# Performance work log

Hardware: AMD Instinct MI355X
Metric: run time of the kernel (lower is better)

The kernel has to match this reference:

```python
import jax, jax.numpy as jnp
import numpy as np

N, E = 100000, 1600000
D_IN, D_HID, D_OUT = 128, 128, 64


def setup_inputs() -> dict:
    key = jax.random.key(0)
    ks = jax.random.split(key, 12)
    x = jax.random.normal(ks[0], (N, D_IN), dtype=jnp.float32)
    edge_index = jax.random.randint(ks[1], (2, E), 0, N, dtype=jnp.int32)

    def glorot(k, fan_in, fan_out):
        lim = np.sqrt(6.0 / (fan_in + fan_out)).astype(np.float32)
        return jax.random.uniform(k, (fan_in, fan_out), jnp.float32, -lim, lim)

    return {
        "x": x,
        "edge_index": edge_index,
        "W_l0": glorot(ks[2], D_IN, D_HID), "W_r0": glorot(ks[3], D_IN, D_HID), "b0": jnp.zeros((D_HID,), jnp.float32),
        "W_l1": glorot(ks[4], D_HID, D_HID), "W_r1": glorot(ks[5], D_HID, D_HID), "b1": jnp.zeros((D_HID,), jnp.float32),
        "W_l2": glorot(ks[6], D_HID, D_OUT), "W_r2": glorot(ks[7], D_HID, D_OUT), "b2": jnp.zeros((D_OUT,), jnp.float32),
    }


def _sage_conv(x, src, dst, W_l, W_r, b):
    # mean aggregation of source features onto destination nodes
    msg = jnp.take(x, src, axis=0)                               # [E, d]
    agg = jax.ops.segment_sum(msg, dst, num_segments=N)          # [N, d]
    deg = jax.ops.segment_sum(jnp.ones_like(dst, x.dtype), dst, num_segments=N)
    agg = agg / jnp.maximum(deg, 1.0)[:, None]
    # out = lin_l(aggr) + lin_r(x); lin_l has bias (PyG SAGEConv convention)
    return agg @ W_l + x @ W_r + b


def reference(x, edge_index, W_l0, W_r0, b0, W_l1, W_r1, b1, W_l2, W_r2, b2):
    src, dst = edge_index[0], edge_index[1]
    h = jax.nn.relu(_sage_conv(x, src, dst, W_l0, W_r0, b0))
    h = jax.nn.relu(_sage_conv(h, src, dst, W_l1, W_r1, b1))
    # dropout is identity in eval mode
    return _sage_conv(h, src, dst, W_l2, W_r2, b2)
```

## Files before the change

### kernel.cpp

```cpp
#include <hip/hip_runtime.h>
#include <hip/hip_bf16.h>
#include <stdint.h>

#define D 128
#define BSH 8
#define BKN 256
#define TILE 4096
#define CAPB 5376

typedef __attribute__((ext_vector_type(8))) short short8;
typedef __attribute__((ext_vector_type(4))) float f32x4;

typedef __attribute__((address_space(1))) const void gvoid;
typedef __attribute__((address_space(3))) void lvoid;

__device__ inline float bf16lo(uint32_t u){ return __uint_as_float(u << 16); }
__device__ inline float bf16hi(uint32_t u){ return __uint_as_float(u & 0xffff0000u); }
__device__ inline unsigned short f2bf(float f){
    union { __hip_bfloat16 h; unsigned short u; } cvt;
    cvt.h = __float2bfloat16(f);
    return cvt.u;
}

#define ACC8(q) \
    acc[0] += bf16lo(q.x); acc[1] += bf16hi(q.x); \
    acc[2] += bf16lo(q.y); acc[3] += bf16hi(q.y); \
    acc[4] += bf16lo(q.z); acc[5] += bf16hi(q.z); \
    acc[6] += bf16lo(q.w); acc[7] += bf16hi(q.w);

__global__ __launch_bounds__(256) void bin_edges(
    const int* __restrict__ src, const int* __restrict__ dst,
    int* __restrict__ bfill, uint32_t* __restrict__ binbuf, int E, int nbk)
{
    __shared__ int hist[400];
    __shared__ int cur[400];
    int t = threadIdx.x;
    int tile0 = blockIdx.x * TILE;
    int cnt = min(TILE, E - tile0);

    for (int i = t; i < nbk; i += 256) hist[i] = 0;
    __syncthreads();
    for (int i = t; i < cnt; i += 256)
        atomicAdd(&hist[dst[tile0 + i] >> BSH], 1);
    __syncthreads();
    for (int i = t; i < nbk; i += 256){
        int h = hist[i];
        int base = h ? atomicAdd(&bfill[i], h) : 0;
        cur[i] = i * CAPB + base;
    }
    __syncthreads();
    for (int i = t; i < cnt; i += 256){
        int d = dst[tile0 + i];
        int b = d >> BSH;
        int p = atomicAdd(&cur[b], 1);
        binbuf[p] = (uint32_t)src[tile0 + i] | ((uint32_t)(d & (BKN - 1)) << 17);
    }
}

__global__ __launch_bounds__(256) void fill_bucket(
    const uint32_t* __restrict__ binbuf, const int* __restrict__ bcnt,
    int* __restrict__ roff, int* __restrict__ rend, int* __restrict__ csr, int n, int nbk)
{
    __shared__ int hist[BKN];
    __shared__ int hist2[BKN];
    __shared__ int hb[BKN];
    __shared__ int sc[256];
    int b = blockIdx.x, t = threadIdx.x;
    int e0 = b * CAPB;
    int e1 = e0 + bcnt[b];
    int v0 = b << BSH;
    int nv = min(BKN, n - v0);

    hist[t] = 0; hist2[t] = 0;
    __syncthreads();
    for (int e = e0 + t; e < e1; e += 256)
        atomicAdd(&hist[binbuf[e] >> 17], 1);
    __syncthreads();
    int own = hist[t];
    sc[t] = own;
    __syncthreads();
    for (int o = 1; o < 256; o <<= 1){
        int x = (t >= o) ? sc[t - o] : 0;
        __syncthreads();
        sc[t] += x;
        __syncthreads();
    }
    int ex = sc[t] - own;
    hb[t] = ex;
    if (t < nv){
        roff[v0 + t] = e0 + ex;
        rend[v0 + t] = e0 + ex + own;
    }
    __syncthreads();
    for (int e = e0 + t; e < e1; e += 256){
        uint32_t p = binbuf[e];
        int local = p >> 17;
        int pos = e0 + hb[local] + atomicAdd(&hist2[local], 1);
        csr[pos] = (int)(p & 0x1FFFFu);
    }
}

__global__ void wt_prep_all(
    const float* __restrict__ Wl0, const float* __restrict__ Wr0,
    const float* __restrict__ Wl1, const float* __restrict__ Wr1,
    const float* __restrict__ Wl2, const float* __restrict__ Wr2,
    unsigned short* __restrict__ WT0, unsigned short* __restrict__ WT1,
    unsigned short* __restrict__ WT2)
{
    int idx = blockIdx.x * 256 + threadIdx.x;
    if (idx < 32768){
        int k = idx & 127, j = idx >> 7;
        WT0[j * 128 + k] = f2bf(j < 128 ? Wl0[k * 128 + j] : Wr0[k * 128 + (j - 128)]);
    } else if (idx < 65536){
        int i = idx - 32768; int k = i & 127, j = i >> 7;
        WT1[j * 128 + k] = f2bf(j < 128 ? Wl1[k * 128 + j] : Wr1[k * 128 + (j - 128)]);
    } else if (idx < 81920){
        int i = idx - 65536; int k = i & 127, j = i >> 7;
        WT2[j * 128 + k] = f2bf(j < 64 ? Wl2[k * 64 + j] : Wr2[k * 64 + (j - 64)]);
    }
}

template<int NC, bool AF32>
__global__ __launch_bounds__(256, 3) void dense_gemm(
    const unsigned short* __restrict__ xb, const float* __restrict__ xf,
    const unsigned short* __restrict__ WT, const float* __restrict__ bias,
    unsigned short* __restrict__ ylz, int n)
{
    constexpr int DOUT = NC / 2;
    __shared__ __align__(16) char As[128 * 256];
    int tid = threadIdx.x, lane = tid & 63, wave = tid >> 6;
    int rbase = blockIdx.x * 128;
    int lrow = lane & 15, lk = (lane >> 4) * 8;
    int colbase = blockIdx.y * 128 + wave * 32;

    short8 bfr[4][2];
    #pragma unroll
    for (int kk = 0; kk < 4; kk++)
        #pragma unroll
        for (int cf = 0; cf < 2; cf++)
            bfr[kk][cf] = *reinterpret_cast<const short8*>(
                WT + (size_t)(colbase + cf * 16 + lrow) * 128 + kk * 32 + lk);

    if constexpr (AF32){
        int cb = (tid & 15) * 16;
        #pragma unroll
        for (int i = 0; i < 8; i++){
            int row = i * 16 + (tid >> 4);
            int grow = min(rbase + row, n - 1);
            const float* p = xf + (size_t)grow * 128 + (cb >> 1);
            float4 f0 = *reinterpret_cast<const float4*>(p);
            float4 f1 = *reinterpret_cast<const float4*>(p + 4);
            uint4 q;
            q.x = (uint32_t)f2bf(f0.x) | ((uint32_t)f2bf(f0.y) << 16);
            q.y = (uint32_t)f2bf(f0.z) | ((uint32_t)f2bf(f0.w) << 16);
            q.z = (uint32_t)f2bf(f1.x) | ((uint32_t)f2bf(f1.y) << 16);
            q.w = (uint32_t)f2bf(f1.z) | ((uint32_t)f2bf(f1.w) << 16);
            *reinterpret_cast<uint4*>(As + row * 256 + (cb ^ ((row & 7) << 4))) = q;
        }
    } else {
        int cb = (lane & 15) * 16;
        #pragma unroll
        for (int i = 0; i < 8; i++){
            int row = i * 16 + (tid >> 4);
            int grow = min(rbase + row, n - 1);
            const unsigned short* gsrc = xb + (size_t)grow * 128 + ((cb ^ ((row & 7) << 4)) >> 1);
            __builtin_amdgcn_global_load_lds(
                (gvoid*)gsrc,
                (lvoid*)(As + (i * 16 + wave * 4) * 256),
                16, 0, 0);
        }
    }
    __syncthreads();

    f32x4 acc[8][2];
    #pragma unroll
    for (int fr = 0; fr < 8; fr++)
        #pragma unroll
        for (int cf = 0; cf < 2; cf++)
            acc[fr][cf] = (f32x4){0.f, 0.f, 0.f, 0.f};

    #pragma unroll
    for (int kk = 0; kk < 4; kk++){
        int cb = kk * 64 + (lane >> 4) * 16;
        #pragma unroll
        for (int fr = 0; fr < 8; fr++){
            int row = fr * 16 + lrow;
            short8 a = *reinterpret_cast<const short8*>(As + row * 256 + (cb ^ ((row & 7) << 4)));
            #pragma unroll
            for (int cf = 0; cf < 2; cf++)
                acc[fr][cf] = __builtin_amdgcn_mfma_f32_16x16x32_bf16(bfr[kk][cf], a, acc[fr][cf], 0, 0, 0);
        }
    }

    float4 bv[2];
    #pragma unroll
    for (int cf = 0; cf < 2; cf++){
        int cg = colbase + cf * 16 + (lane >> 4) * 4;
        bv[cf] = (cg >= DOUT) ? *reinterpret_cast<const float4*>(bias + (cg - DOUT))
                              : (float4){0.f, 0.f, 0.f, 0.f};
    }

    #pragma unroll
    for (int fr = 0; fr < 8; fr++){
        int row = rbase + fr * 16 + lrow;
        if (row < n){
            #pragma unroll
            for (int cf = 0; cf < 2; cf++){
                int cg = colbase + cf * 16 + (lane >> 4) * 4;
                uint2 o;
                o.x = (uint32_t)f2bf(acc[fr][cf][0] + bv[cf].x) |
                      ((uint32_t)f2bf(acc[fr][cf][1] + bv[cf].y) << 16);
                o.y = (uint32_t)f2bf(acc[fr][cf][2] + bv[cf].z) |
                      ((uint32_t)f2bf(acc[fr][cf][3] + bv[cf].w) << 16);
                *reinterpret_cast<uint2*>(ylz + (size_t)row * NC + cg) = o;
            }
        }
    }
}

__global__ __launch_bounds__(256, 4) void agg_relu(
    const unsigned short* __restrict__ ylz, const int* __restrict__ roff,
    const int* __restrict__ rend,
    const int* __restrict__ csr, unsigned short* __restrict__ hout, int n)
{
    int grp = threadIdx.x >> 4, li = threadIdx.x & 15;
    int v = blockIdx.x * 16 + grp;
    if (v >= n) return;
    int s0 = roff[v], s1 = rend[v];
    const unsigned short* base = ylz + li * 8;
    float acc[8] = {0.f,0.f,0.f,0.f,0.f,0.f,0.f,0.f};
    int e = s0;
    for (; e + 8 <= s1; e += 8){
        int i0=csr[e],i1=csr[e+1],i2=csr[e+2],i3=csr[e+3];
        int i4=csr[e+4],i5=csr[e+5],i6=csr[e+6],i7=csr[e+7];
        uint4 q0 = *reinterpret_cast<const uint4*>(base + (size_t)i0 * 256);
        uint4 q1 = *reinterpret_cast<const uint4*>(base + (size_t)i1 * 256);
        uint4 q2 = *reinterpret_cast<const uint4*>(base + (size_t)i2 * 256);
        uint4 q3 = *reinterpret_cast<const uint4*>(base + (size_t)i3 * 256);
        uint4 q4 = *reinterpret_cast<const uint4*>(base + (size_t)i4 * 256);
        uint4 q5 = *reinterpret_cast<const uint4*>(base + (size_t)i5 * 256);
        uint4 q6 = *reinterpret_cast<const uint4*>(base + (size_t)i6 * 256);
        uint4 q7 = *reinterpret_cast<const uint4*>(base + (size_t)i7 * 256);
        ACC8(q0) ACC8(q1) ACC8(q2) ACC8(q3) ACC8(q4) ACC8(q5) ACC8(q6) ACC8(q7)
    }
    if (e < s1){
        int last = s1 - 1;
        int i0=csr[e];
        int i1=csr[min(e+1,last)],i2=csr[min(e+2,last)],i3=csr[min(e+3,last)];
        int i4=csr[min(e+4,last)],i5=csr[min(e+5,last)],i6=csr[min(e+6,last)],i7=csr[min(e+7,last)];
        uint4 z4 = make_uint4(0,0,0,0);
        uint4 q0 = *reinterpret_cast<const uint4*>(base + (size_t)i0 * 256);
        uint4 q1 = *reinterpret_cast<const uint4*>(base + (size_t)i1 * 256);
        uint4 q2 = *reinterpret_cast<const uint4*>(base + (size_t)i2 * 256);
        uint4 q3 = *reinterpret_cast<const uint4*>(base + (size_t)i3 * 256);
        uint4 q4 = *reinterpret_cast<const uint4*>(base + (size_t)i4 * 256);
        uint4 q5 = *reinterpret_cast<const uint4*>(base + (size_t)i5 * 256);
        uint4 q6 = *reinterpret_cast<const uint4*>(base + (size_t)i6 * 256);
        uint4 q7 = *reinterpret_cast<const uint4*>(base + (size_t)i7 * 256);
        if (e+1 > last) q1 = z4;
        if (e+2 > last) q2 = z4;
        if (e+3 > last) q3 = z4;
        if (e+4 > last) q4 = z4;
        if (e+5 > last) q5 = z4;
        if (e+6 > last) q6 = z4;
        if (e+7 > last) q7 = z4;
        ACC8(q0) ACC8(q1) ACC8(q2) ACC8(q3) ACC8(q4) ACC8(q5) ACC8(q6) ACC8(q7)
    }
    int d = s1 - s0;
    float inv = (d > 0) ? 1.0f / (float)d : 0.0f;
    uint4 zq = *reinterpret_cast<const uint4*>(ylz + (size_t)v * 256 + 128 + li * 8);
    float z0=bf16lo(zq.x), z1=bf16hi(zq.x), z2=bf16lo(zq.y), z3=bf16hi(zq.y);
    float z4_=bf16lo(zq.z), z5=bf16hi(zq.z), z6=bf16lo(zq.w), z7=bf16hi(zq.w);
    uint4 o;
    o.x = (uint32_t)f2bf(fmaxf(acc[0]*inv+z0,0.f)) | ((uint32_t)f2bf(fmaxf(acc[1]*inv+z1,0.f)) << 16);
    o.y = (uint32_t)f2bf(fmaxf(acc[2]*inv+z2,0.f)) | ((uint32_t)f2bf(fmaxf(acc[3]*inv+z3,0.f)) << 16);
    o.z = (uint32_t)f2bf(fmaxf(acc[4]*inv+z4_,0.f)) | ((uint32_t)f2bf(fmaxf(acc[5]*inv+z5,0.f)) << 16);
    o.w = (uint32_t)f2bf(fmaxf(acc[6]*inv+z6,0.f)) | ((uint32_t)f2bf(fmaxf(acc[7]*inv+z7,0.f)) << 16);
    *reinterpret_cast<uint4*>(hout + (size_t)v * 128 + li * 8) = o;
}

__global__ __launch_bounds__(256, 4) void agg_out64(
    const unsigned short* __restrict__ ylz, const int* __restrict__ roff,
    const int* __restrict__ rend,
    const int* __restrict__ csr, float* __restrict__ out, int n)
{
    int grp = threadIdx.x >> 3, li = threadIdx.x & 7;
    int v = blockIdx.x * 32 + grp;
    if (v >= n) return;
    int s0 = roff[v], s1 = rend[v];
    const unsigned short* base = ylz + li * 8;
    float acc[8] = {0.f,0.f,0.f,0.f,0.f,0.f,0.f,0.f};
    int e = s0;
    for (; e + 8 <= s1; e += 8){
        int i0=csr[e],i1=csr[e+1],i2=csr[e+2],i3=csr[e+3];
        int i4=csr[e+4],i5=csr[e+5],i6=csr[e+6],i7=csr[e+7];
        uint4 q0 = *reinterpret_cast<const uint4*>(base + (size_t)i0 * 128);
        uint4 q1 = *reinterpret_cast<const uint4*>(base + (size_t)i1 * 128);
        uint4 q2 = *reinterpret_cast<const uint4*>(base + (size_t)i2 * 128);
        uint4 q3 = *reinterpret_cast<const uint4*>(base + (size_t)i3 * 128);
        uint4 q4 = *reinterpret_cast<const uint4*>(base + (size_t)i4 * 128);
        uint4 q5 = *reinterpret_cast<const uint4*>(base + (size_t)i5 * 128);
        uint4 q6 = *reinterpret_cast<const uint4*>(base + (size_t)i6 * 128);
        uint4 q7 = *reinterpret_cast<const uint4*>(base + (size_t)i7 * 128);
        ACC8(q0) ACC8(q1) ACC8(q2) ACC8(q3) ACC8(q4) ACC8(q5) ACC8(q6) ACC8(q7)
    }
    if (e < s1){
        int last = s1 - 1;
        int i0=csr[e];
        int i1=csr[min(e+1,last)],i2=csr[min(e+2,last)],i3=csr[min(e+3,last)];
        int i4=csr[min(e+4,last)],i5=csr[min(e+5,last)],i6=csr[min(e+6,last)],i7=csr[min(e+7,last)];
        uint4 z4 = make_uint4(0,0,0,0);
        uint4 q0 = *reinterpret_cast<const uint4*>(base + (size_t)i0 * 128);
        uint4 q1 = *reinterpret_cast<const uint4*>(base + (size_t)i1 * 128);
        uint4 q2 = *reinterpret_cast<const uint4*>(base + (size_t)i2 * 128);
        uint4 q3 = *reinterpret_cast<const uint4*>(base + (size_t)i3 * 128);
        uint4 q4 = *reinterpret_cast<const uint4*>(base + (size_t)i4 * 128);
        uint4 q5 = *reinterpret_cast<const uint4*>(base + (size_t)i5 * 128);
        uint4 q6 = *reinterpret_cast<const uint4*>(base + (size_t)i6 * 128);
        uint4 q7 = *reinterpret_cast<const uint4*>(base + (size_t)i7 * 128);
        if (e+1 > last) q1 = z4;
        if (e+2 > last) q2 = z4;
        if (e+3 > last) q3 = z4;
        if (e+4 > last) q4 = z4;
        if (e+5 > last) q5 = z4;
        if (e+6 > last) q6 = z4;
        if (e+7 > last) q7 = z4;
        ACC8(q0) ACC8(q1) ACC8(q2) ACC8(q3) ACC8(q4) ACC8(q5) ACC8(q6) ACC8(q7)
    }
    int d = s1 - s0;
    float inv = (d > 0) ? 1.0f / (float)d : 0.0f;
    uint4 zq = *reinterpret_cast<const uint4*>(ylz + (size_t)v * 128 + 64 + li * 8);
    float4 o0, o1;
    o0.x = acc[0]*inv + bf16lo(zq.x);
    o0.y = acc[1]*inv + bf16hi(zq.x);
    o0.z = acc[2]*inv + bf16lo(zq.y);
    o0.w = acc[3]*inv + bf16hi(zq.y);
    o1.x = acc[4]*inv + bf16lo(zq.z);
    o1.y = acc[5]*inv + bf16hi(zq.z);
    o1.z = acc[6]*inv + bf16lo(zq.w);
    o1.w = acc[7]*inv + bf16hi(zq.w);
    *reinterpret_cast<float4*>(out + (size_t)v * 64 + li * 8) = o0;
    *reinterpret_cast<float4*>(out + (size_t)v * 64 + li * 8 + 4) = o1;
}

extern "C" void kernel_launch(void* const* d_in, const int* in_sizes, int n_in,
                              void* d_out, int out_size, void* d_ws, size_t ws_size,
                              hipStream_t stream)
{
    const float* x   = (const float*)d_in[0];
    const int*   ei  = (const int*)d_in[1];
    const float* Wl0 = (const float*)d_in[2];
    const float* Wr0 = (const float*)d_in[3];
    const float* b0  = (const float*)d_in[4];
    const float* Wl1 = (const float*)d_in[5];
    const float* Wr1 = (const float*)d_in[6];
    const float* b1  = (const float*)d_in[7];
    const float* Wl2 = (const float*)d_in[8];
    const float* Wr2 = (const float*)d_in[9];
    const float* b2  = (const float*)d_in[10];

    int N = in_sizes[0] / D;
    int E = in_sizes[1] / 2;
    const int* src = ei;
    const int* dst = ei + E;
    int NBK = (N + BKN - 1) >> BSH;

    char* ws = (char*)d_ws;
    size_t off = 0;
    auto alloc = [&](size_t bytes) -> void* {
        void* p = ws + off;
        off = (off + bytes + 255) & ~(size_t)255;
        return p;
    };
    int*      bfill  = (int*)alloc((size_t)NBK * 4);
    int*      roff   = (int*)alloc((size_t)N * 4);
    int*      rend   = (int*)alloc((size_t)N * 4);
    int*      csr    = (int*)alloc((size_t)NBK * CAPB * 4);
    unsigned short* ylz = (unsigned short*)alloc((size_t)N * 256 * 2);
    unsigned short* h0  = (unsigned short*)alloc((size_t)N * D * 2);
    unsigned short* h1  = (unsigned short*)alloc((size_t)N * D * 2);
    unsigned short* WT0 = (unsigned short*)alloc((size_t)256 * 128 * 2);
    unsigned short* WT1 = (unsigned short*)alloc((size_t)256 * 128 * 2);
    unsigned short* WT2 = (unsigned short*)alloc((size_t)128 * 128 * 2);
    uint32_t* binbuf = (uint32_t*)ylz;

    hipMemsetAsync(bfill, 0, (size_t)NBK * 4, stream);

    bin_edges<<<(E + TILE - 1) / TILE, 256, 0, stream>>>(src, dst, bfill, binbuf, E, NBK);
    fill_bucket<<<NBK, 256, 0, stream>>>(binbuf, bfill, roff, rend, csr, N, NBK);

    wt_prep_all<<<320, 256, 0, stream>>>(Wl0, Wr0, Wl1, Wr1, Wl2, Wr2, WT0, WT1, WT2);

    int gG = (N + 127) / 128;
    int gA = (N + 15) / 16;
    int gA2 = (N + 31) / 32;

    dense_gemm<256, true ><<<dim3(gG, 2), 256, 0, stream>>>(nullptr, x, WT0, b0, ylz, N);
    agg_relu<<<gA, 256, 0, stream>>>(ylz, roff, rend, csr, h0, N);
    dense_gemm<256, false><<<dim3(gG, 2), 256, 0, stream>>>(h0, nullptr, WT1, b1, ylz, N);
    agg_relu<<<gA, 256, 0, stream>>>(ylz, roff, rend, csr, h1, N);
    dense_gemm<128, false><<<dim3(gG, 1), 256, 0, stream>>>(h1, nullptr, WT2, b2, ylz, N);
    agg_out64<<<gA2, 256, 0, stream>>>(ylz, roff, rend, csr, (float*)d_out, N);
}
```

Measured before the change: 275.9 us.

## Merge independent preprocessing kernels to cut launch count and overlap work

Fuses edge binning with weight transposition into one launch, and the CSR bucket fill with the first-layer GEMM into another, using block-index ranges to dispatch roles. Binbuf gets its own workspace allocation so the GEMM can write ylz while the fill reads binbuf. This removes two kernel launches and lets independent work share the GPU. In exchange it uses more workspace memory, and the fused kernels carry heterogeneous blocks with shared LDS sizing.

```diff
diff --git a/kernel.cpp b/kernel.cpp
--- a/kernel.cpp
+++ b/kernel.cpp
@@ -28,110 +28,111 @@
     acc[4] += bf16lo(q.z); acc[5] += bf16hi(q.z); \
     acc[6] += bf16lo(q.w); acc[7] += bf16hi(q.w);
 
-__global__ __launch_bounds__(256) void bin_edges(
+__global__ __launch_bounds__(256) void prep_and_bin(
     const int* __restrict__ src, const int* __restrict__ dst,
-    int* __restrict__ bfill, uint32_t* __restrict__ binbuf, int E, int nbk)
-{
-    __shared__ int hist[400];
-    __shared__ int cur[400];
-    int t = threadIdx.x;
-    int tile0 = blockIdx.x * TILE;
-    int cnt = min(TILE, E - tile0);
-
-    for (int i = t; i < nbk; i += 256) hist[i] = 0;
-    __syncthreads();
-    for (int i = t; i < cnt; i += 256)
-        atomicAdd(&hist[dst[tile0 + i] >> BSH], 1);
-    __syncthreads();
-    for (int i = t; i < nbk; i += 256){
-        int h = hist[i];
-        int base = h ? atomicAdd(&bfill[i], h) : 0;
-        cur[i] = i * CAPB + base;
-    }
-    __syncthreads();
-    for (int i = t; i < cnt; i += 256){
-        int d = dst[tile0 + i];
-        int b = d >> BSH;
-        int p = atomicAdd(&cur[b], 1);
-        binbuf[p] = (uint32_t)src[tile0 + i] | ((uint32_t)(d & (BKN - 1)) << 17);
-    }
-}
-
-__global__ __launch_bounds__(256) void fill_bucket(
-    const uint32_t* __restrict__ binbuf, const int* __restrict__ bcnt,
-    int* __restrict__ roff, int* __restrict__ rend, int* __restrict__ csr, int n, int nbk)
-{
-    __shared__ int hist[BKN];
-    __shared__ int hist2[BKN];
-    __shared__ int hb[BKN];
-    __shared__ int sc[256];
-    int b = blockIdx.x, t = threadIdx.x;
-    int e0 = b * CAPB;
-    int e1 = e0 + bcnt[b];
-    int v0 = b << BSH;
-    int nv = min(BKN, n - v0);
-
-    hist[t] = 0; hist2[t] = 0;
-    __syncthreads();
-    for (int e = e0 + t; e < e1; e += 256)
-        atomicAdd(&hist[binbuf[e] >> 17], 1);
-    __syncthreads();
-    int own = hist[t];
-    sc[t] = own;
-    __syncthreads();
-    for (int o = 1; o < 256; o <<= 1){
-        int x = (t >= o) ? sc[t - o] : 0;
-        __syncthreads();
-        sc[t] += x;
-        __syncthreads();
-    }
-    int ex = sc[t] - own;
-    hb[t] = ex;
-    if (t < nv){
-        roff[v0 + t] = e0 + ex;
-        rend[v0 + t] = e0 + ex + own;
-    }
-    __syncthreads();
-    for (int e = e0 + t; e < e1; e += 256){
-        uint32_t p = binbuf[e];
-        int local = p >> 17;
-        int pos = e0 + hb[local] + atomicAdd(&hist2[local], 1);
-        csr[pos] = (int)(p & 0x1FFFFu);
-    }
-}
-
-__global__ void wt_prep_all(
+    int* __restrict__ bfill, uint32_t* __restrict__ binbuf, int E, int nbk, int nBin,
     const float* __restrict__ Wl0, const float* __restrict__ Wr0,
     const float* __restrict__ Wl1, const float* __restrict__ Wr1,
     const float* __restrict__ Wl2, const float* __restrict__ Wr2,
     unsigned short* __restrict__ WT0, unsigned short* __restrict__ WT1,
     unsigned short* __restrict__ WT2)
 {
-    int idx = blockIdx.x * 256 + threadIdx.x;
-    if (idx < 32768){
-        int k = idx & 127, j = idx >> 7;
-        WT0[j * 128 + k] = f2bf(j < 128 ? Wl0[k * 128 + j] : Wr0[k * 128 + (j - 128)]);
-    } else if (idx < 65536){
-        int i = idx - 32768; int k = i & 127, j = i >> 7;
-        WT1[j * 128 + k] = f2bf(j < 128 ? Wl1[k * 128 + j] : Wr1[k * 128 + (j - 128)]);
-    } else if (idx < 81920){
-        int i = idx - 65536; int k = i & 127, j = i >> 7;
-        WT2[j * 128 + k] = f2bf(j < 64 ? Wl2[k * 64 + j] : Wr2[k * 64 + (j - 64)]);
-    }
-}
-
-template<int NC, bool AF32>
-__global__ __launch_bounds__(256, 3) void dense_gemm(
-    const unsigned short* __restrict__ xb, const float* __restrict__ xf,
-    const unsigned short* __restrict__ WT, const float* __restrict__ bias,
-    unsigned short* __restrict__ ylz, int n)
-{
-    constexpr int DOUT = NC / 2;
-    __shared__ __align__(16) char As[128 * 256];
-    int tid = threadIdx.x, lane = tid & 63, wave = tid >> 6;
-    int rbase = blockIdx.x * 128;
+    __shared__ int hist[400];
+    __shared__ int cur[400];
+    int t = threadIdx.x;
+    if ((int)blockIdx.x < nBin){
+        int tile0 = blockIdx.x * TILE;
+        int cnt = min(TILE, E - tile0);
+        for (int i = t; i < nbk; i += 256) hist[i] = 0;
+        __syncthreads();
+        for (int i = t; i < cnt; i += 256)
+            atomicAdd(&hist[dst[tile0 + i] >> BSH], 1);
+        __syncthreads();
+        for (int i = t; i < nbk; i += 256){
+            int h = hist[i];
+            int base = h ? atomicAdd(&bfill[i], h) : 0;
+            cur[i] = i * CAPB + base;
+        }
+        __syncthreads();
+        for (int i = t; i < cnt; i += 256){
+            int d = dst[tile0 + i];
+            int b = d >> BSH;
+            int p = atomicAdd(&cur[b], 1);
+            binbuf[p] = (uint32_t)src[tile0 + i] | ((uint32_t)(d & (BKN - 1)) << 17);
+        }
+    } else {
+        int idx = ((int)blockIdx.x - nBin) * 256 + t;
+        if (idx < 32768){
+            int k = idx & 127, j = idx >> 7;
+            WT0[j * 128 + k] = f2bf(j < 128 ? Wl0[k * 128 + j] : Wr0[k * 128 + (j - 128)]);
+        } else if (idx < 65536){
+            int i = idx - 32768; int k = i & 127, j = i >> 7;
+            WT1[j * 128 + k] = f2bf(j < 128 ? Wl1[k * 128 + j] : Wr1[k * 128 + (j - 128)]);
+        } else if (idx < 81920){
+            int i = idx - 65536; int k = i & 127, j = i >> 7;
+            WT2[j * 128 + k] = f2bf(j < 64 ? Wl2[k * 64 + j] : Wr2[k * 64 + (j - 64)]);
+        }
+    }
+}
+
+__global__ __launch_bounds__(256, 3) void gemm0_fill(
+    const float* __restrict__ xf, const unsigned short* __restrict__ WT,
+    const float* __restrict__ bias, unsigned short* __restrict__ ylz, int n,
+    const uint32_t* __restrict__ binbuf, const int* __restrict__ bcnt,
+    int* __restrict__ roff, int* __restrict__ rend, int* __restrict__ csr,
+    int nbk, int gG)
+{
+    __shared__ __align__(16) char smem[128 * 256];
+    int tid = threadIdx.x;
+
+    if ((int)blockIdx.x < nbk){
+        int* hist  = (int*)smem;
+        int* hist2 = hist + 256;
+        int* hb    = hist2 + 256;
+        int* sc    = hb + 256;
+        int b = blockIdx.x, t = tid;
+        int e0 = b * CAPB;
+        int e1 = e0 + bcnt[b];
+        int v0 = b << BSH;
+        int nv = min(BKN, n - v0);
+
+        hist[t] = 0; hist2[t] = 0;
+        __syncthreads();
+        for (int e = e0 + t; e < e1; e += 256)
+            atomicAdd(&hist[binbuf[e] >> 17], 1);
+        __syncthreads();
+        int own = hist[t];
+        sc[t] = own;
+        __syncthreads();
+        for (int o = 1; o < 256; o <<= 1){
+            int x = (t >= o) ? sc[t - o] : 0;
+            __syncthreads();
+            sc[t] += x;
+            __syncthreads();
+        }
+        int ex = sc[t] - own;
+        hb[t] = ex;
+        if (t < nv){
+            roff[v0 + t] = e0 + ex;
+            rend[v0 + t] = e0 + ex + own;
+        }
+        __syncthreads();
+        for (int e = e0 + t; e < e1; e += 256){
+            uint32_t p = binbuf[e];
+            int local = p >> 17;
+            int pos = e0 + hb[local] + atomicAdd(&hist2[local], 1);
+            csr[pos] = (int)(p & 0x1FFFFu);
+        }
+        return;
+    }
+
+    int bid = (int)blockIdx.x - nbk;
+    int bx = bid % gG, by = bid / gG;
+    char* As = smem;
+    int lane = tid & 63, wave = tid >> 6;
+    int rbase = bx * 128;
     int lrow = lane & 15, lk = (lane >> 4) * 8;
-    int colbase = blockIdx.y * 128 + wave * 32;
+    int colbase = by * 128 + wave * 32;
 
     short8 bfr[4][2];
     #pragma unroll
@@ -141,7 +142,7 @@
             bfr[kk][cf] = *reinterpret_cast<const short8*>(
                 WT + (size_t)(colbase + cf * 16 + lrow) * 128 + kk * 32 + lk);
 
-    if constexpr (AF32){
+    {
         int cb = (tid & 15) * 16;
         #pragma unroll
         for (int i = 0; i < 8; i++){
@@ -157,7 +158,77 @@
             q.w = (uint32_t)f2bf(f1.z) | ((uint32_t)f2bf(f1.w) << 16);
             *reinterpret_cast<uint4*>(As + row * 256 + (cb ^ ((row & 7) << 4))) = q;
         }
-    } else {
+    }
+    __syncthreads();
+
+    f32x4 acc[8][2];
+    #pragma unroll
+    for (int fr = 0; fr < 8; fr++)
+        #pragma unroll
+        for (int cf = 0; cf < 2; cf++)
+            acc[fr][cf] = (f32x4){0.f, 0.f, 0.f, 0.f};
+
+    #pragma unroll
+    for (int kk = 0; kk < 4; kk++){
+        int cb = kk * 64 + (lane >> 4) * 16;
+        #pragma unroll
+        for (int fr = 0; fr < 8; fr++){
+            int row = fr * 16 + lrow;
+            short8 a = *reinterpret_cast<const short8*>(As + row * 256 + (cb ^ ((row & 7) << 4)));
+            #pragma unroll
+            for (int cf = 0; cf < 2; cf++)
+                acc[fr][cf] = __builtin_amdgcn_mfma_f32_16x16x32_bf16(bfr[kk][cf], a, acc[fr][cf], 0, 0, 0);
+        }
+    }
+
+    float4 bv[2];
+    #pragma unroll
+    for (int cf = 0; cf < 2; cf++){
+        int cg = colbase + cf * 16 + (lane >> 4) * 4;
+        bv[cf] = (cg >= 128) ? *reinterpret_cast<const float4*>(bias + (cg - 128))
+                             : (float4){0.f, 0.f, 0.f, 0.f};
+    }
+
+    #pragma unroll
+    for (int fr = 0; fr < 8; fr++){
+        int row = rbase + fr * 16 + lrow;
+        if (row < n){
+            #pragma unroll
+            for (int cf = 0; cf < 2; cf++){
+                int cg = colbase + cf * 16 + (lane >> 4) * 4;
+                uint2 o;
+                o.x = (uint32_t)f2bf(acc[fr][cf][0] + bv[cf].x) |
+                      ((uint32_t)f2bf(acc[fr][cf][1] + bv[cf].y) << 16);
+                o.y = (uint32_t)f2bf(acc[fr][cf][2] + bv[cf].z) |
+                      ((uint32_t)f2bf(acc[fr][cf][3] + bv[cf].w) << 16);
+                *reinterpret_cast<uint2*>(ylz + (size_t)row * 256 + cg) = o;
+            }
+        }
+    }
+}
+
+template<int NC>
+__global__ __launch_bounds__(256, 3) void dense_gemm(
+    const unsigned short* __restrict__ xb,
+    const unsigned short* __restrict__ WT, const float* __restrict__ bias,
+    unsigned short* __restrict__ ylz, int n)
+{
+    constexpr int DOUT = NC / 2;
+    __shared__ __align__(16) char As[128 * 256];
+    int tid = threadIdx.x, lane = tid & 63, wave = tid >> 6;
+    int rbase = blockIdx.x * 128;
+    int lrow = lane & 15, lk = (lane >> 4) * 8;
+    int colbase = blockIdx.y * 128 + wave * 32;
+
+    short8 bfr[4][2];
+    #pragma unroll
+    for (int kk = 0; kk < 4; kk++)
+        #pragma unroll
+        for (int cf = 0; cf < 2; cf++)
+            bfr[kk][cf] = *reinterpret_cast<const short8*>(
+                WT + (size_t)(colbase + cf * 16 + lrow) * 128 + kk * 32 + lk);
+
+    {
         int cb = (lane & 15) * 16;
         #pragma unroll
         for (int i = 0; i < 8; i++){
@@ -382,23 +453,25 @@
     unsigned short* WT0 = (unsigned short*)alloc((size_t)256 * 128 * 2);
     unsigned short* WT1 = (unsigned short*)alloc((size_t)256 * 128 * 2);
     unsigned short* WT2 = (unsigned short*)alloc((size_t)128 * 128 * 2);
-    uint32_t* binbuf = (uint32_t*)ylz;
+    uint32_t* binbuf = (uint32_t*)alloc((size_t)NBK * CAPB * 4);
 
     hipMemsetAsync(bfill, 0, (size_t)NBK * 4, stream);
 
-    bin_edges<<<(E + TILE - 1) / TILE, 256, 0, stream>>>(src, dst, bfill, binbuf, E, NBK);
-    fill_bucket<<<NBK, 256, 0, stream>>>(binbuf, bfill, roff, rend, csr, N, NBK);
-
-    wt_prep_all<<<320, 256, 0, stream>>>(Wl0, Wr0, Wl1, Wr1, Wl2, Wr2, WT0, WT1, WT2);
-
+    int nBin = (E + TILE - 1) / TILE;
     int gG = (N + 127) / 128;
     int gA = (N + 15) / 16;
     int gA2 = (N + 31) / 32;
 
-    dense_gemm<256, true ><<<dim3(gG, 2), 256, 0, stream>>>(nullptr, x, WT0, b0, ylz, N);
+    prep_and_bin<<<nBin + 320, 256, 0, stream>>>(
+        src, dst, bfill, binbuf, E, NBK, nBin,
+        Wl0, Wr0, Wl1, Wr1, Wl2, Wr2, WT0, WT1, WT2);
+
+    gemm0_fill<<<NBK + gG * 2, 256, 0, stream>>>(
+        x, WT0, b0, ylz, N, binbuf, bfill, roff, rend, csr, NBK, gG);
+
     agg_relu<<<gA, 256, 0, stream>>>(ylz, roff, rend, csr, h0, N);
-    dense_gemm<256, false><<<dim3(gG, 2), 256, 0, stream>>>(h0, nullptr, WT1, b1, ylz, N);
+    dense_gemm<256><<<dim3(gG, 2), 256, 0, stream>>>(h0, WT1, b1, ylz, N);
     agg_relu<<<gA, 256, 0, stream>>>(ylz, roff, rend, csr, h1, N);
-    dense_gemm<128, false><<<dim3(gG, 1), 256, 0, stream>>>(h1, nullptr, WT2, b2, ylz, N);
+    dense_gemm<128><<<dim3(gG, 1), 256, 0, stream>>>(h1, WT2, b2, ylz, N);
     agg_out64<<<gA2, 256, 0, stream>>>(ylz, roff, rend, csr, (float*)d_out, N);
 }
```

After: 262.9 us (median of 2 runs). 4.7% less time.
